# Kernel tuning notes

Measured on AMD Instinct MI355X. Metric: run time of the kernel, lower is better.

Reference implementation:

```python
import jax, jax.numpy as jnp
import numpy as np

K = 16  # nsample for knn_point

def _bn(x, g, b):
    # inference-mode BatchNorm1d folded to per-channel affine (running stats 0/1)
    return x * g[None, :, None] + b[None, :, None]

def _knn(xyz, k):
    # xyz: [B,3,N] -> idx [B,N,k] of k nearest neighbors (squared L2)
    p = xyz.transpose(0, 2, 1)                                   # [B,N,3]
    sq = jnp.sum(p * p, axis=-1)                                 # [B,N]
    d = sq[:, :, None] + sq[:, None, :] - 2.0 * jnp.einsum('bnc,bmc->bnm', p, p)
    _, idx = jax.lax.top_k(-d, k)
    return idx

def _gather(hT, idx):
    # hT: [B,N,C], idx: [B,N,K] -> [B,N,K,C]
    return jax.vmap(lambda a, i: a[i])(hT, idx)

def setup_inputs():
    key = jax.random.key(0)
    ks = jax.random.split(key, 12)
    B, N, C = 16, 2048, 128
    def w(k, shape, fan):
        return jax.random.normal(k, shape, jnp.float32) * (1.0 / np.sqrt(fan))
    o = jnp.ones; z = jnp.zeros
    return {
        'points': jax.random.normal(ks[0], (B, 6, N), jnp.float32),
        'label': jax.random.uniform(ks[1], (B, 1, 16), jnp.float32),
        'We1': w(ks[2], (C, 6), 6), 'ge1': o(C), 'be1': z(C),
        'We2': w(ks[3], (C, C), C), 'ge2': o(C), 'be2': z(C),
        'W1': w(ks[4], (3, C, C), C), 'g1': o((3, C)), 'b1': z((3, C)),
        'W2': w(ks[5], (3, C, C), C), 'g2': o((3, C)), 'b2': z((3, C)),
        'Wf': w(ks[6], (1024, 3 * C), 3 * C), 'gf': o(1024), 'bf': z(1024),
        'Wl': w(ks[7], (64, 16), 16), 'gl': o(64), 'bl': z(64),
        'Wc1': w(ks[8], (512, 3136), 3136), 'bc1': z(512), 'gc1': o(512), 'bb1': z(512),
        'Wc2': w(ks[9], (256, 512), 512), 'bc2': z(256), 'gc2': o(256), 'bb2': z(256),
        'Wc3': w(ks[10], (50, 256), 256), 'bc3': z(50),
    }

def reference(points, label, We1, ge1, be1, We2, ge2, be2, W1, g1, b1, W2, g2, b2,
              Wf, gf, bf, Wl, gl, bl, Wc1, bc1, gc1, bb1, Wc2, bc2, gc2, bb2, Wc3, bc3):
    B, _, N = points.shape
    x = points[:, :6, :]
    xyz = x[:, :3, :]
    idx = _knn(xyz, K)                                            # [B,N,16]
    # input embedding: two conv1x1 + BN + ReLU
    h = jax.nn.relu(_bn(jnp.einsum('oc,bcn->bon', We1, x), ge1, be1))
    h = jax.nn.relu(_bn(jnp.einsum('oc,bcn->bon', We2, h), ge2, be2))
    xs = []
    for i in range(3):  # PVDSA_Res blocks (simplified: conv-BN-ReLU, kNN max-agg, conv-BN + residual)
        t = jax.nn.relu(_bn(jnp.einsum('oc,bcn->bon', W1[i], h), g1[i], b1[i]))
        nbr = _gather(t.transpose(0, 2, 1), idx)                  # [B,N,K,C]
        m = nbr.max(axis=2).transpose(0, 2, 1)                    # [B,C,N]
        h = jax.nn.relu(_bn(jnp.einsum('oc,bcn->bon', W2[i], m), g2[i], b2[i]) + h)
        xs.append(h)
    xcat = jnp.concatenate(xs, axis=1)                            # [B,384,N]
    xf = jax.nn.leaky_relu(_bn(jnp.einsum('oc,bcn->bon', Wf, xcat), gf, bf), 0.2)  # [B,1024,N]
    x_max = xf.max(axis=-1)                                       # [B,1024]
    x_avg = xf.mean(axis=-1)                                      # [B,1024]
    cls = jnp.broadcast_to(label.transpose(0, 2, 1), (B, 16, N))
    lab = jax.nn.leaky_relu(_bn(jnp.einsum('oc,bcn->bon', Wl, cls), gl, bl), 0.2)  # [B,64,N]
    glob = jnp.concatenate([
        jnp.broadcast_to(x_max[:, :, None], (B, 1024, N)),
        jnp.broadcast_to(x_avg[:, :, None], (B, 1024, N)),
        lab], axis=1)
    xa = jnp.concatenate([xf, glob], axis=1)                      # [B,3136,N]
    c = jax.nn.relu(_bn(jnp.einsum('oc,bcn->bon', Wc1, xa) + bc1[None, :, None], gc1, bb1))
    c = jax.nn.relu(_bn(jnp.einsum('oc,bcn->bon', Wc2, c) + bc2[None, :, None], gc2, bb2))
    out = jnp.einsum('oc,bcn->bon', Wc3, c) + bc3[None, :, None]  # [B,50,N]
    return out
```

## Files before the change

kernel.cpp:

```cpp
#include <hip/hip_runtime.h>
#include <cstdint>
#include <cstddef>

#define DEVINL __device__ __forceinline__

typedef float    f32x4 __attribute__((ext_vector_type(4)));
typedef _Float16 f16x8 __attribute__((ext_vector_type(8)));
typedef _Float16 f16x4 __attribute__((ext_vector_type(4)));
typedef short    s16x8 __attribute__((ext_vector_type(8)));

constexpr int BB = 16, NN = 2048, MM = 32768;

constexpr size_t OFF_WE1 = 0;
constexpr size_t OFF_WE2 = OFF_WE1 + 128 * 64 * 2;
constexpr size_t OFF_W1  = OFF_WE2 + 128 * 128 * 2;
constexpr size_t OFF_W2  = OFF_W1  + 3 * 128 * 128 * 2;
constexpr size_t OFF_WF  = OFF_W2  + 3 * 128 * 128 * 2;
constexpr size_t OFF_WC1 = OFF_WF  + 1024 * 384 * 2;
constexpr size_t OFF_WC2 = OFF_WC1 + 512 * 1024 * 2;
constexpr size_t OFF_WC3 = OFF_WC2 + 256 * 512 * 2;
constexpr size_t OFF_BC2 = OFF_WC3 + 128 * 256 * 2;
constexpr size_t OFF_BC3 = OFF_BC2 + 256 * 4;
constexpr size_t OFF_CVEC= OFF_BC3 + 128 * 4;
constexpr size_t OFF_PMAX= OFF_CVEC+ 16 * 512 * 4;
// ... 450 lines not shown
    for (int a = 0; a < 4; ++a)
#pragma unroll
        for (int c = 0; c < 2; ++c) acc1[a][c] = (f32x4){0.f, 0.f, 0.f, 0.f};
#pragma unroll
    for (int kt = 0; kt < 2; ++kt)
#pragma unroll
        for (int ks = 0; ks < 2; ++ks) {
            f16x8 af[4], bf[2];
#pragma unroll
            for (int oi = 0; oi < 4; ++oi) {
                const int row = oh + oi * 16 + r;
                const int slot = (ks * 4 + quad) ^ (row & 7);
                af[oi] = *(const f16x8*)(Aa + kt * 8192 + row * 64 + slot * 8);
            }
#pragma unroll
            for (int mi = 0; mi < 2; ++mi) {
                const int row = mh + mi * 16 + r;
                const int slot = (ks * 4 + quad) ^ (row & 7);
                bf[mi] = *(const f16x8*)(Bm + kt * 4096 + row * 64 + slot * 8);
            }
#pragma unroll
            for (int oi = 0; oi < 4; ++oi)
#pragma unroll
                for (int mi = 0; mi < 2; ++mi)
                    acc1[oi][mi] = __builtin_amdgcn_mfma_f32_16x16x32_f16(af[oi], bf[mi], acc1[oi][mi], 0, 0, 0);
        }
    __syncthreads();

    if constexpr (HAS_G2) {
#pragma unroll
        for (int kt = 0; kt < 2; ++kt)
#pragma unroll
            for (int t = 0; t < 4; ++t) {
                const int row = t * 32 + srow;
                const int gk = kt * 64 + ((sslot ^ (row & 7)) << 3);
                __builtin_amdgcn_global_load_lds(
                    (const __attribute__((address_space(1))) unsigned int*)(Wb + (size_t)row * 128 + gk),
                    (__attribute__((address_space(3))) unsigned int*)(Ab + kt * 8192 + t * 2048 + wave * 512),
                    16, 0, 0);
            }
    }

#pragma unroll
    for (int oi = 0; oi < 4; ++oi) {
        const int ol = oh + oi * 16 + quad * 4;
        const f32x4 bv = *(const f32x4*)(ba + ol);
        const int kt = ol >> 6, kk = ol & 63;
        const int chunk = kk >> 3, within = kk & 7;
#pragma unroll
        for (int mi = 0; mi < 2; ++mi) {
            const int row = mh + mi * 16 + r;
            f32x4 v = acc1[oi][mi] + bv;
            f16x4 rr = *(const f16x4*)(Res + (size_t)(m_blk + row) * ldR + roff + ol);
#pragma unroll
            for (int j = 0; j < 4; ++j) v[j] += (float)rr[j];
            f16x4 ov;
#pragma unroll
            for (int j = 0; j < 4; ++j) { float x = v[j]; ov[j] = (_Float16)((x > 0.f) ? x : 0.f); }
            *(f16x4*)(By1 + kt * 4096 + row * 64 + ((chunk ^ (row & 7)) << 3) + within) = ov;
        }
    }
    __syncthreads();

#pragma unroll
    for (int it = 0; it < 4; ++it) {
        const int g = it * 256 + tid;
        const int row = g >> 4, c = g & 15;
        const int kt = c >> 3, cc = c & 7;
        f16x8 o8 = *(const f16x8*)(By1 + kt * 4096 + row * 64 + ((cc ^ (row & 7)) << 3));
        *(f16x8*)(Y1 + (size_t)(m_blk + row) * 384 + yoff1 + c * 8) = o8;
    }

    if constexpr (HAS_G2) {
        f32x4 acc2[4][2];
#pragma unroll
        for (int a = 0; a < 4; ++a)
#pragma unroll
            for (int c = 0; c < 2; ++c) acc2[a][c] = (f32x4){0.f, 0.f, 0.f, 0.f};
#pragma unroll
        for (int kt = 0; kt < 2; ++kt)
#pragma unroll
            for (int ks = 0; ks < 2; ++ks) {
                f16x8 af[4], bf[2];
#pragma unroll
                for (int oi = 0; oi < 4; ++oi) {
                    const int row = oh + oi * 16 + r;
                    const int slot = (ks * 4 + quad) ^ (row & 7);
                    af[oi] = *(const f16x8*)(Ab + kt * 8192 + row * 64 + slot * 8);
                }
#pragma unroll
                for (int mi = 0; mi < 2; ++mi) {
                    const int row = mh + mi * 16 + r;
                    const int slot = (ks * 4 + quad) ^ (row & 7);
                    bf[mi] = *(const f16x8*)(By1 + kt * 4096 + row * 64 + slot * 8);
                }
#pragma unroll
                for (int oi = 0; oi < 4; ++oi)
#pragma unroll
                    for (int mi = 0; mi < 2; ++mi)
                        acc2[oi][mi] = __builtin_amdgcn_mfma_f32_16x16x32_f16(af[oi], bf[mi], acc2[oi][mi], 0, 0, 0);
            }

#pragma unroll
        for (int oi = 0; oi < 4; ++oi) {
            const int ol = oh + oi * 16 + quad * 4;
            const f32x4 bv = *(const f32x4*)(bb + ol);
#pragma unroll
            for (int mi = 0; mi < 2; ++mi) {
                const int row = mh + mi * 16 + r;
                f32x4 v = acc2[oi][mi] + bv;
                f16x4 ov;
#pragma unroll
                for (int j = 0; j < 4; ++j) { float x = v[j]; ov[j] = (_Float16)((x > 0.f) ? x : 0.f); }
                const int s = ((ol >> 2) ^ (row & 31)) << 2;
                *(f16x4*)(OT2 + row * 128 + s) = ov;
            }
        }
        __syncthreads();
#pragma unroll
        for (int it2 = 0; it2 < 4; ++it2) {
            const int row = it2 * 16 + (tid >> 4);
            const int c = tid & 15;
            const int s0 = ((c * 2) ^ (row & 31)) << 2;
            const int s1 = ((c * 2 + 1) ^ (row & 31)) << 2;
            f16x4 a  = *(const f16x4*)(OT2 + row * 128 + s0);
            f16x4 b2 = *(const f16x4*)(OT2 + row * 128 + s1);
            f16x8 o8;
            o8[0] = a[0]; o8[1] = a[1]; o8[2] = a[2]; o8[3] = a[3];
            o8[4] = b2[0]; o8[5] = b2[1]; o8[6] = b2[2]; o8[7] = b2[3];
            *(f16x8*)(Y2 + (size_t)(m_blk + row) * 128 + c * 8) = o8;
        }
    }
}

__global__ __launch_bounds__(256) void c2c3_kernel(
    const _Float16* __restrict__ W2c, const _Float16* __restrict__ W3c,
    const _Float16* __restrict__ X, float* __restrict__ Y32,
    const float* __restrict__ b2v, const float* __restrict__ b3v)
{
    __shared__ _Float16 SH[36864];
    _Float16* As = SH;
    _Float16* Bs = SH + 16384;
    _Float16* Y1 = SH + 20480;

    const int tid = threadIdx.x;
    const int lane = tid & 63, w = tid >> 6;
    const int r = lane & 15, quad = lane >> 4;
    const int m_blk = blockIdx.x * 64;

    const int srow  = w * 8 + (lane >> 3);
    const int sslot = lane & 7;

    f32x4 acc1[4][4];
#pragma unroll
    for (int a = 0; a < 4; ++a)
#pragma unroll
        for (int c = 0; c < 4; ++c) acc1[a][c] = (f32x4){0.f, 0.f, 0.f, 0.f};

    for (int kt8 = 0; kt8 < 8; ++kt8) {
        const int k0 = kt8 << 6;
        __syncthreads();
#pragma unroll
        for (int t = 0; t < 8; ++t) {
            const int row = t * 32 + srow;
            const int gk = k0 + ((sslot ^ (row & 7)) << 3);
            __builtin_amdgcn_global_load_lds(
                (const __attribute__((address_space(1))) unsigned int*)(W2c + (size_t)row * 512 + gk),
                (__attribute__((address_space(3))) unsigned int*)(As + t * 2048 + w * 512),
                16, 0, 0);
        }
#pragma unroll
        for (int t = 0; t < 2; ++t) {
            const int row = t * 32 + srow;
            const int gk = k0 + ((sslot ^ (row & 7)) << 3);
            __builtin_amdgcn_global_load_lds(
                (const __attribute__((address_space(1))) unsigned int*)(X + (size_t)(m_blk + row) * 512 + gk),
                (__attribute__((address_space(3))) unsigned int*)(Bs + t * 2048 + w * 512),
                16, 0, 0);
        }
        __syncthreads();
#pragma unroll
        for (int ks = 0; ks < 2; ++ks) {
            f16x8 af[4], bf[4];
#pragma unroll
            for (int oi = 0; oi < 4; ++oi) {
                const int row = w * 64 + oi * 16 + r;
                const int slot = (ks * 4 + quad) ^ (row & 7);
                af[oi] = *(const f16x8*)(As + row * 64 + slot * 8);
            }
#pragma unroll
            for (int mi = 0; mi < 4; ++mi) {
                const int row = mi * 16 + r;
                const int slot = (ks * 4 + quad) ^ (row & 7);
                bf[mi] = *(const f16x8*)(Bs + row * 64 + slot * 8);
            }
#pragma unroll
            for (int oi = 0; oi < 4; ++oi)
#pragma unroll
                for (int mi = 0; mi < 4; ++mi)
                    acc1[oi][mi] = __builtin_amdgcn_mfma_f32_16x16x32_f16(af[oi], bf[mi], acc1[oi][mi], 0, 0, 0);
        }
    }
    __syncthreads();

#pragma unroll
    for (int kk2 = 0; kk2 < 2; ++kk2)
#pragma unroll
        for (int t = 0; t < 4; ++t) {
            const int row = t * 32 + srow;
            const int gk = (kk2 << 6) + ((sslot ^ (row & 7)) << 3);
            __builtin_amdgcn_global_load_lds(
                (const __attribute__((address_space(1))) unsigned int*)(W3c + (size_t)row * 256 + gk),
                (__attribute__((address_space(3))) unsigned int*)(As + kk2 * 8192 + t * 2048 + w * 512),
                16, 0, 0);
        }

#pragma unroll
    for (int oi = 0; oi < 4; ++oi) {
        const int ol = w * 64 + oi * 16 + quad * 4;
        const f32x4 bv = *(const f32x4*)(b2v + ol);
        const int kk = ol & 63;
        const int chunk = kk >> 3, within = kk & 7;
#pragma unroll
        for (int mi = 0; mi < 4; ++mi) {
            const int row = mi * 16 + r;
            f32x4 v = acc1[oi][mi] + bv;
            f16x4 ov;
#pragma unroll
            for (int j = 0; j < 4; ++j) { float x = v[j]; ov[j] = (_Float16)((x > 0.f) ? x : 0.f); }
            *(f16x4*)(Y1 + w * 4096 + row * 64 + ((chunk ^ (row & 7)) << 3) + within) = ov;
        }
    }
    __syncthreads();

    f32x4 acc2[2][4];
#pragma unroll
    for (int a = 0; a < 2; ++a)
#pragma unroll
        for (int c = 0; c < 4; ++c) acc2[a][c] = (f32x4){0.f, 0.f, 0.f, 0.f};

#pragma unroll
    for (int h = 0; h < 2; ++h) {
        if (h == 1) {
            __syncthreads();
#pragma unroll
            for (int kk2 = 0; kk2 < 2; ++kk2)
#pragma unroll
                for (int t = 0; t < 4; ++t) {
                    const int row = t * 32 + srow;
                    const int gk = ((2 + kk2) << 6) + ((sslot ^ (row & 7)) << 3);
                    __builtin_amdgcn_global_load_lds(
                        (const __attribute__((address_space(1))) unsigned int*)(W3c + (size_t)row * 256 + gk),
                        (__attribute__((address_space(3))) unsigned int*)(As + kk2 * 8192 + t * 2048 + w * 512),
                        16, 0, 0);
                }
            __syncthreads();
        }
#pragma unroll
        for (int kk2 = 0; kk2 < 2; ++kk2) {
            const int kt = h * 2 + kk2;
#pragma unroll
            for (int ks = 0; ks < 2; ++ks) {
                f16x8 af2[2], bf2[4];
#pragma unroll
                for (int oi2 = 0; oi2 < 2; ++oi2) {
                    const int row = w * 32 + oi2 * 16 + r;
                    const int slot = (ks * 4 + quad) ^ (row & 7);
                    af2[oi2] = *(const f16x8*)(As + kk2 * 8192 + row * 64 + slot * 8);
                }
#pragma unroll
                for (int mi = 0; mi < 4; ++mi) {
                    const int row = mi * 16 + r;
                    const int slot = (ks * 4 + quad) ^ (row & 7);
                    bf2[mi] = *(const f16x8*)(Y1 + kt * 4096 + row * 64 + slot * 8);
                }
#pragma unroll
                for (int oi2 = 0; oi2 < 2; ++oi2)
#pragma unroll
                    for (int mi = 0; mi < 4; ++mi)
                        acc2[oi2][mi] = __builtin_amdgcn_mfma_f32_16x16x32_f16(af2[oi2], bf2[mi], acc2[oi2][mi], 0, 0, 0);
            }
        }
    }

#pragma unroll
    for (int oi2 = 0; oi2 < 2; ++oi2) {
        const int og = w * 32 + oi2 * 16 + quad * 4;
        const f32x4 bv = *(const f32x4*)(b3v + og);
#pragma unroll
        for (int mi = 0; mi < 4; ++mi) {
            const int m = m_blk + mi * 16 + r;
            const int bidx = m >> 11, n = m & 2047;
            f32x4 v = acc2[oi2][mi] + bv;
#pragma unroll
            for (int j = 0; j < 4; ++j) {
                const int o = og + j;
                if (o < 50)
                    Y32[((size_t)(bidx * 50 + o) << 11) + n] = v[j];
            }
        }
    }
}

__global__ __launch_bounds__(512, 2) void gemm256(
    const _Float16* __restrict__ W, const _Float16* __restrict__ X,
    _Float16* __restrict__ Y, const float* __restrict__ bias,
    int Kp, int ldX, int ldY, int Opad, int act, int biasPerBatch,
    float* __restrict__ pmax, float* __restrict__ psum)
{
    constexpr int ASZ = 256 * 64;
    __shared__ _Float16 SH[65536];
    const int tid  = threadIdx.x;
    const int lane = tid & 63, wave = tid >> 6;
    const int r = lane & 15, quad = lane >> 4;
    const int wo = wave & 3, wm = wave >> 2;
    const int m_blk = blockIdx.x * 256, o_blk = blockIdx.y * 256;
    const int nt = Kp >> 6;

    f32x4 acc[4][8];
#pragma unroll
    for (int a = 0; a < 4; ++a)
#pragma unroll
        for (int c = 0; c < 8; ++c) acc[a][c] = (f32x4){0.f, 0.f, 0.f, 0.f};

    const int srow  = wave * 8 + (lane >> 3);
    const int sslot = lane & 7;

    auto STAGE = [&](int bufi, int k0) {
        _Float16* As = SH + bufi * (2 * ASZ);
        _Float16* Bs = As + ASZ;
#pragma unroll
        for (int t = 0; t < 4; ++t) {
            const int rowA = t * 64 + srow;
            const int gk = k0 + ((sslot ^ (rowA & 7)) << 3);
            const _Float16* gA = W + (size_t)(o_blk + rowA) * Kp + gk;
            __builtin_amdgcn_global_load_lds(
                (const __attribute__((address_space(1))) unsigned int*)gA,
                (__attribute__((address_space(3))) unsigned int*)(As + t * 4096 + wave * 512),
                16, 0, 0);
        }
#pragma unroll
        for (int t = 0; t < 4; ++t) {
            const int rowB = t * 64 + srow;
            const int gk = k0 + ((sslot ^ (rowB & 7)) << 3);
            const _Float16* gB = X + (size_t)(m_blk + rowB) * ldX + gk;
            __builtin_amdgcn_global_load_lds(
                (const __attribute__((address_space(1))) unsigned int*)gB,
                (__attribute__((address_space(3))) unsigned int*)(Bs + t * 4096 + wave * 512),
                16, 0, 0);
        }
    };

    STAGE(0, 0);
    int cur = 0;
    for (int t = 0; t < nt; ++t) {
        if (t + 1 < nt) {
            STAGE(cur ^ 1, (t + 1) << 6);
            asm volatile("s_waitcnt vmcnt(8)" ::: "memory");
        } else {
            asm volatile("s_waitcnt vmcnt(0)" ::: "memory");
        }
        __builtin_amdgcn_sched_barrier(0);
        __builtin_amdgcn_s_barrier();
        asm volatile("" ::: "memory");

        const _Float16* As = SH + cur * (2 * ASZ);
        const _Float16* Bs = As + ASZ;
        __builtin_amdgcn_s_setprio(1);
#pragma unroll
        for (int ks = 0; ks < 2; ++ks) {
            f16x8 af[4], bf[8];
#pragma unroll
            for (int oi = 0; oi < 4; ++oi) {
                const int row = (wo << 6) + (oi << 4) + r;
                const int slot = (ks * 4 + quad) ^ (row & 7);
                af[oi] = *(const f16x8*)(As + row * 64 + slot * 8);
            }
#pragma unroll
            for (int mi = 0; mi < 8; ++mi) {
                const int row = (wm << 7) + (mi << 4) + r;
                const int slot = (ks * 4 + quad) ^ (row & 7);
                bf[mi] = *(const f16x8*)(Bs + row * 64 + slot * 8);
            }
#pragma unroll
            for (int oi = 0; oi < 4; ++oi)
#pragma unroll
                for (int mi = 0; mi < 8; ++mi)
                    acc[oi][mi] = __builtin_amdgcn_mfma_f32_16x16x32_f16(af[oi], bf[mi], acc[oi][mi], 0, 0, 0);
        }
        __builtin_amdgcn_s_setprio(0);
        asm volatile("" ::: "memory");
        __builtin_amdgcn_s_barrier();
        cur ^= 1;
    }
    __syncthreads();

    const int bb = biasPerBatch ? (m_blk >> 11) * Opad : 0;
    _Float16* OT = SH;
#pragma unroll
    for (int oi = 0; oi < 4; ++oi) {
        const int ol = (wo << 6) + (oi << 4) + (quad << 2);
        const f32x4 bv = *(const f32x4*)(bias + bb + o_blk + ol);
#pragma unroll
        for (int mi = 0; mi < 8; ++mi) {
            const int row = (wm << 7) + (mi << 4) + r;
            f32x4 v = acc[oi][mi] + bv;
            f16x4 ov;
#pragma unroll
            for (int j = 0; j < 4; ++j) {
                float x = v[j];
                if (act == 1)      x = (x > 0.f) ? x : 0.0f;
                else if (act == 2) x = (x > 0.f) ? x : 0.2f * x;
                ov[j] = (_Float16)x;
            }
            const int s = (ol >> 2) ^ (row & 31);
            *(f16x4*)(OT + row * 256 + s * 4) = ov;
        }
    }
    __syncthreads();
#pragma unroll
    for (int p2 = 0; p2 < 16; ++p2) {
        const int g = (p2 << 9) + tid;
        const int row = g >> 5, c = g & 31;
        const int s0 = ((c << 1)) ^ (row & 31);
        const int s1 = ((c << 1) | 1) ^ (row & 31);
        f16x4 a  = *(const f16x4*)(OT + row * 256 + s0 * 4);
        f16x4 b2 = *(const f16x4*)(OT + row * 256 + s1 * 4);
        f16x8 o8;
        o8[0] = a[0]; o8[1] = a[1]; o8[2] = a[2]; o8[3] = a[3];
        o8[4] = b2[0]; o8[5] = b2[1]; o8[6] = b2[2]; o8[7] = b2[3];
        *(f16x8*)(Y + (size_t)(m_blk + row) * ldY + o_blk + (c << 3)) = o8;
    }

    if (pmax) {
        const int cg = tid & 63, h8 = tid >> 6;
        float mx0 = -3.4e38f, mx1 = -3.4e38f, mx2 = -3.4e38f, mx3 = -3.4e38f;
        float sm0 = 0.f, sm1 = 0.f, sm2 = 0.f, sm3 = 0.f;
#pragma unroll
        for (int rr = 0; rr < 32; ++rr) {
            const int row = (h8 << 5) + rr;
            const f16x4 v = *(const f16x4*)(OT + row * 256 + ((cg ^ (row & 31)) << 2));
            const float x0 = (float)v[0], x1 = (float)v[1], x2 = (float)v[2], x3 = (float)v[3];
            mx0 = fmaxf(mx0, x0); sm0 += x0;
            mx1 = fmaxf(mx1, x1); sm1 += x1;
            mx2 = fmaxf(mx2, x2); sm2 += x2;
            mx3 = fmaxf(mx3, x3); sm3 += x3;
        }
        __syncthreads();
        float* PR = (float*)SH;
        float* pw = PR + (size_t)(((h8 << 8) + (cg << 2)) << 1);
        pw[0] = mx0; pw[1] = sm0; pw[2] = mx1; pw[3] = sm1;
        pw[4] = mx2; pw[5] = sm2; pw[6] = mx3; pw[7] = sm3;
        __syncthreads();
        if (tid < 256) {
            float M = -3.4e38f, S = 0.f;
#pragma unroll
            for (int h2 = 0; h2 < 8; ++h2) {
                M = fmaxf(M, PR[(size_t)(((h2 << 8) + tid) << 1)]);
                S += PR[(size_t)(((h2 << 8) + tid) << 1) + 1];
            }
            const int b2 = m_blk >> 11, mt = (m_blk >> 8) & 7;
            pmax[((size_t)((b2 << 3) + mt) << 10) + o_blk + tid] = M;
            psum[((size_t)((b2 << 3) + mt) << 10) + o_blk + tid] = S;
        }
    }
}

template<int TM>
__global__ __launch_bounds__(256) void gemm_tile(
    const _Float16* __restrict__ W, const _Float16* __restrict__ X,
    _Float16* __restrict__ Y, float* __restrict__ Y32,
    const float* __restrict__ bias, const _Float16* __restrict__ Res,
    int Kp, int ldX, int xoff, int ldY, int yoff, int Opad,
    int act, int biasPerBatch, int ldR, int roff, int Olimit)
{
    constexpr int MI = TM / 32;
    constexpr int ASZ = 128 * 64;
    constexpr int BSZ = TM * 64;
    __shared__ _Float16 SH[2 * (ASZ + BSZ)];

    const int tid  = threadIdx.x;
    const int lane = tid & 63, wave = tid >> 6;
    const int r = lane & 15, quad = lane >> 4;
    const int m_blk = blockIdx.x * TM, o_blk = blockIdx.y * 128;
    const int oh = (wave >> 1) * 64, mh = (wave & 1) * (TM / 2);

    f32x4 acc[4][MI];
#pragma unroll
    for (int a = 0; a < 4; ++a)
#pragma unroll
        for (int c = 0; c < MI; ++c) acc[a][c] = (f32x4){0.f, 0.f, 0.f, 0.f};

    const int srow  = wave * 8 + (lane >> 3);
    const int sslot = lane & 7;

    auto STAGE = [&](int bufi, int k0) {
        _Float16* As = SH + bufi * (ASZ + BSZ);
        _Float16* Bs = As + ASZ;
#pragma unroll
        for (int t = 0; t < 4; ++t) {
            const int rowA = t * 32 + srow;
            const int gk = k0 + ((sslot ^ (rowA & 7)) << 3);
            const _Float16* gA = W + (size_t)(o_blk + rowA) * Kp + gk;
            __builtin_amdgcn_global_load_lds(
                (const __attribute__((address_space(1))) unsigned int*)gA,
                (__attribute__((address_space(3))) unsigned int*)(As + t * 2048 + wave * 512),
                16, 0, 0);
        }
#pragma unroll
        for (int t = 0; t < TM / 32; ++t) {
            const int rowB = t * 32 + srow;
            const int gk = k0 + ((sslot ^ (rowB & 7)) << 3);
            const _Float16* gB = X + (size_t)(m_blk + rowB) * ldX + xoff + gk;
            __builtin_amdgcn_global_load_lds(
                (const __attribute__((address_space(1))) unsigned int*)gB,
                (__attribute__((address_space(3))) unsigned int*)(Bs + t * 2048 + wave * 512),
                16, 0, 0);
        }
    };

    const int nt = Kp >> 6;
    STAGE(0, 0);
    int cur = 0;
    for (int t = 0; t < nt; ++t) {
        if (t + 1 < nt) {
            STAGE(cur ^ 1, (t + 1) << 6);
            if constexpr (TM == 128) asm volatile("s_waitcnt vmcnt(8)" ::: "memory");
            else                     asm volatile("s_waitcnt vmcnt(6)" ::: "memory");
        } else {
            asm volatile("s_waitcnt vmcnt(0)" ::: "memory");
        }
        __builtin_amdgcn_sched_barrier(0);
        __builtin_amdgcn_s_barrier();
        asm volatile("" ::: "memory");

        const _Float16* As = SH + cur * (ASZ + BSZ);
        const _Float16* Bs = As + ASZ;
        __builtin_amdgcn_s_setprio(1);
#pragma unroll
        for (int ks = 0; ks < 2; ++ks) {
            f16x8 af[4], bf[MI];
#pragma unroll
            for (int oi = 0; oi < 4; ++oi) {
                const int row = oh + oi * 16 + r;
                const int slot = (ks * 4 + quad) ^ (row & 7);
                af[oi] = *(const f16x8*)(As + row * 64 + slot * 8);
            }
#pragma unroll
            for (int mi = 0; mi < MI; ++mi) {
                const int row = mh + mi * 16 + r;
                const int slot = (ks * 4 + quad) ^ (row & 7);
                bf[mi] = *(const f16x8*)(Bs + row * 64 + slot * 8);
            }
#pragma unroll
            for (int oi = 0; oi < 4; ++oi)
#pragma unroll
                for (int mi = 0; mi < MI; ++mi)
                    acc[oi][mi] = __builtin_amdgcn_mfma_f32_16x16x32_f16(af[oi], bf[mi], acc[oi][mi], 0, 0, 0);
        }
        __builtin_amdgcn_s_setprio(0);
        asm volatile("" ::: "memory");
        __builtin_amdgcn_s_barrier();
        cur ^= 1;
    }

    const int bb = biasPerBatch ? (m_blk >> 11) * Opad : 0;
    __syncthreads();

    if (Y32) {
#pragma unroll
        for (int oi = 0; oi < 4; ++oi) {
            const int og = o_blk + oh + oi * 16 + quad * 4;
            const f32x4 bv = *(const f32x4*)(bias + bb + og);
#pragma unroll
            for (int mi = 0; mi < MI; ++mi) {
                const int m = m_blk + mh + mi * 16 + r;
                const int bidx = m >> 11, n = m & 2047;
                f32x4 v = acc[oi][mi] + bv;
#pragma unroll
                for (int j = 0; j < 4; ++j) {
                    float x = v[j];
                    if (act == 1)      x = (x > 0.f) ? x : 0.0f;
                    else if (act == 2) x = (x > 0.f) ? x : 0.2f * x;
                    const int o = og + j;
                    if (o < Olimit)
                        Y32[((size_t)(bidx * 50 + o) << 11) + n] = x;
                }
            }
        }
        return;
    }

    _Float16* OT = SH;
#pragma unroll
    for (int oi = 0; oi < 4; ++oi) {
        const int ol = oh + oi * 16 + quad * 4;
        const f32x4 bv = *(const f32x4*)(bias + bb + o_blk + ol);
#pragma unroll
        for (int mi = 0; mi < MI; ++mi) {
            const int row = mh + mi * 16 + r;
            f32x4 v = acc[oi][mi] + bv;
            if (Res) {
                f16x4 rr = *(const f16x4*)(Res + (size_t)(m_blk + row) * ldR + roff + o_blk + ol);
#pragma unroll
                for (int j = 0; j < 4; ++j) v[j] += (float)rr[j];
            }
            f16x4 ov;
#pragma unroll
            for (int j = 0; j < 4; ++j) {
                float x = v[j];
                if (act == 1)      x = (x > 0.f) ? x : 0.0f;
                else if (act == 2) x = (x > 0.f) ? x : 0.2f * x;
                ov[j] = (_Float16)x;
            }
            const int s = ((ol >> 2) ^ (row & 31)) << 2;
            *(f16x4*)(OT + row * 128 + s) = ov;
        }
    }
    __syncthreads();
#pragma unroll
    for (int it2 = 0; it2 < TM / 16; ++it2) {
        const int row = it2 * 16 + (tid >> 4);
        const int c = tid & 15;
        const int s0 = ((c * 2) ^ (row & 31)) << 2;
        const int s1 = ((c * 2 + 1) ^ (row & 31)) << 2;
        f16x4 a = *(const f16x4*)(OT + row * 128 + s0);
        f16x4 b2 = *(const f16x4*)(OT + row * 128 + s1);
        f16x8 o8;
        o8[0] = a[0]; o8[1] = a[1]; o8[2] = a[2]; o8[3] = a[3];
        o8[4] = b2[0]; o8[5] = b2[1]; o8[6] = b2[2]; o8[7] = b2[3];
        *(f16x8*)(Y + (size_t)(m_blk + row) * ldY + yoff + o_blk + c * 8) = o8;
    }
}

__global__ __launch_bounds__(256) void cvec_kernel(
    const float* __restrict__ label, const float* __restrict__ Wl, const float* __restrict__ gl, const float* __restrict__ bl,
    const float* __restrict__ Wc1, const float* __restrict__ bc1, const float* __restrict__ gc1, const float* __restrict__ bb1,
    const float* __restrict__ pmax, const float* __restrict__ psum, float* __restrict__ cvec)
{
    __shared__ float v[2112];
    __shared__ float red[256];
    const int b = blockIdx.x, og = blockIdx.y, tid = threadIdx.x;
    for (int i = tid; i < 1024; i += 256) {
        float mx = -3.4e38f, sm = 0.f;
#pragma unroll
        for (int c = 0; c < 8; ++c) {
            mx = fmaxf(mx, pmax[((size_t)(b * 8 + c) << 10) + i]);
            sm += psum[((size_t)(b * 8 + c) << 10) + i];
        }
        v[i] = mx;
        v[1024 + i] = sm * (1.f / 2048.f);
    }
    if (tid < 64) {
        float s = 0.f;
        for (int i = 0; i < 16; ++i) s += Wl[tid * 16 + i] * label[b * 16 + i];
        s = gl[tid] * s + bl[tid];
        v[2048 + tid] = (s > 0.f) ? s : 0.2f * s;
    }
    __syncthreads();
    const int o = og * 64 + (tid >> 2), part = tid & 3;
    const float* wrow = Wc1 + (size_t)o * 3136 + 1024 + part * 528;
    float s = 0.f;
    for (int j = 0; j < 528; ++j) s += wrow[j] * v[part * 528 + j];
    red[tid] = s;
    __syncthreads();
    if (part == 0) {
        float tot = red[tid] + red[tid + 1] + red[tid + 2] + red[tid + 3];
        cvec[((size_t)b << 9) + o] = gc1[o] * (tot + bc1[o]) + bb1[o];
    }
}

extern "C" void kernel_launch(void* const* d_in, const int* in_sizes, int n_in,
                              void* d_out, int out_size, void* d_ws, size_t ws_size,
                              hipStream_t stream)
{
    (void)in_sizes; (void)n_in; (void)out_size; (void)ws_size;
    const float* points = (const float*)d_in[0];
    const float* label  = (const float*)d_in[1];
    const float* We1 = (const float*)d_in[2];
    const float* ge1 = (const float*)d_in[3];
    const float* be1 = (const float*)d_in[4];
    const float* We2 = (const float*)d_in[5];
    const float* ge2 = (const float*)d_in[6];
    const float* be2 = (const float*)d_in[7];
    const float* W1  = (const float*)d_in[8];
    const float* g1  = (const float*)d_in[9];
    const float* b1  = (const float*)d_in[10];
    const float* W2  = (const float*)d_in[11];
    const float* g2  = (const float*)d_in[12];
    const float* b2  = (const float*)d_in[13];
    const float* Wf  = (const float*)d_in[14];
    const float* gf  = (const float*)d_in[15];
    const float* bfv = (const float*)d_in[16];
    const float* Wl  = (const float*)d_in[17];
    const float* gl  = (const float*)d_in[18];
    const float* bl  = (const float*)d_in[19];
    const float* Wc1 = (const float*)d_in[20];
    const float* bc1 = (const float*)d_in[21];
    const float* gc1 = (const float*)d_in[22];
    const float* bb1 = (const float*)d_in[23];
    const float* Wc2 = (const float*)d_in[24];
    const float* bc2 = (const float*)d_in[25];
    const float* gc2 = (const float*)d_in[26];
    const float* bb2 = (const float*)d_in[27];
    const float* Wc3 = (const float*)d_in[28];
    const float* bc3 = (const float*)d_in[29];

    char* ws = (char*)d_ws;
    _Float16* hT  = (_Float16*)(ws + OFF_HT);
    _Float16* tT  = (_Float16*)(ws + OFF_TT);
    _Float16* tT2 = (_Float16*)(ws + OFF_MT);
    _Float16* xct = (_Float16*)(ws + OFF_XCAT);
    _Float16* xf  = (_Float16*)(ws + OFF_XF);
    _Float16* c1  = (_Float16*)(ws + OFF_C1);
    int*      idx = (int*)     (ws + OFF_IDX);
    _Float16* x0  = (_Float16*)(ws + OFF_X0);

    _Float16* wE1 = (_Float16*)(ws + OFF_WE1);
    _Float16* wE2 = (_Float16*)(ws + OFF_WE2);
    _Float16* w1f = (_Float16*)(ws + OFF_W1);
    _Float16* w2f = (_Float16*)(ws + OFF_W2);
    _Float16* wF  = (_Float16*)(ws + OFF_WF);
    _Float16* wC1 = (_Float16*)(ws + OFF_WC1);
    _Float16* wC2 = (_Float16*)(ws + OFF_WC2);
    _Float16* wC3 = (_Float16*)(ws + OFF_WC3);
    float* bC2 = (float*)(ws + OFF_BC2);
    float* bC3 = (float*)(ws + OFF_BC3);
    float* cv  = (float*)(ws + OFF_CVEC);
    float* pmx = (float*)(ws + OFF_PMAX);
    float* psm = (float*)(ws + OFF_PSUM);

    fold_all_kernel<<<dim3(4834), 256, 0, stream>>>(We1, ge1, We2, ge2, W1, g1, W2, g2,
                                                    Wf, gf, Wc1, gc1, Wc2, gc2, Wc3,
                                                    gc2, bc2, bb2, bc3, points, ws);
    knn_kernel<<<dim3(BB, NN / 32), 256, 0, stream>>>(points, idx);

    e12_kernel<<<dim3(512), 256, 0, stream>>>(wE1, wE2, x0, hT, be1, be2);

    gemm_tile<64><<<dim3(512, 1), 256, 0, stream>>>(w1f, hT, tT, nullptr, b1, nullptr,
                                                    128, 128, 0, 128, 0, 128, 1, 0, 0, 0, 128);

    pairg_kernel<true><<<dim3(512), 256, 0, stream>>>(w2f, w1f + 16384, (const short*)tT, idx, hT,
                                                      xct, tT2, b2, b1 + 128, 128, 0, 0);

    pairg_kernel<true><<<dim3(512), 256, 0, stream>>>(w2f + 16384, w1f + 2 * 16384, (const short*)tT2, idx, xct,
                                                      xct, tT, b2 + 128, b1 + 256, 384, 0, 128);

    pairg_kernel<false><<<dim3(512), 256, 0, stream>>>(w2f + 2 * 16384, nullptr, (const short*)tT, idx, xct,
                                                       xct, nullptr, b2 + 256, nullptr, 384, 128, 256);

    gemm256<<<dim3(128, 4), 512, 0, stream>>>(wF, xct, xf, bfv, 384, 384, 1024, 1024, 2, 0, pmx, psm);

    cvec_kernel<<<dim3(BB, 8), 256, 0, stream>>>(label, Wl, gl, bl, Wc1, bc1, gc1, bb1, pmx, psm, cv);

    gemm256<<<dim3(128, 2), 512, 0, stream>>>(wC1, xf, c1, cv, 1024, 1024, 512, 512, 1, 1, nullptr, nullptr);
// ... 4 lines not shown
```

Baseline: 366.7 us.

## Single-buffer gemm256 LDS and split epilogue to raise occupancy

```diff
diff --git a/kernel.cpp b/kernel.cpp
--- a/kernel.cpp
+++ b/kernel.cpp
@@ -776,14 +776,14 @@
     }
 }
 
-__global__ __launch_bounds__(512, 2) void gemm256(
+__global__ __launch_bounds__(512, 4) void gemm256(
     const _Float16* __restrict__ W, const _Float16* __restrict__ X,
     _Float16* __restrict__ Y, const float* __restrict__ bias,
     int Kp, int ldX, int ldY, int Opad, int act, int biasPerBatch,
     float* __restrict__ pmax, float* __restrict__ psum)
 {
     constexpr int ASZ = 256 * 64;
-    __shared__ _Float16 SH[65536];
+    __shared__ _Float16 SH[32768];
     const int tid  = threadIdx.x;
     const int lane = tid & 63, wave = tid >> 6;
     const int r = lane & 15, quad = lane >> 4;
@@ -799,48 +799,33 @@
 
     const int srow  = wave * 8 + (lane >> 3);
     const int sslot = lane & 7;
-
-    auto STAGE = [&](int bufi, int k0) {
-        _Float16* As = SH + bufi * (2 * ASZ);
-        _Float16* Bs = As + ASZ;
-#pragma unroll
-        for (int t = 0; t < 4; ++t) {
-            const int rowA = t * 64 + srow;
+    _Float16* As = SH;
+    _Float16* Bs = SH + ASZ;
+
+    for (int t = 0; t < nt; ++t) {
+        const int k0 = t << 6;
+        __syncthreads();
+#pragma unroll
+        for (int tt = 0; tt < 4; ++tt) {
+            const int rowA = tt * 64 + srow;
             const int gk = k0 + ((sslot ^ (rowA & 7)) << 3);
             const _Float16* gA = W + (size_t)(o_blk + rowA) * Kp + gk;
             __builtin_amdgcn_global_load_lds(
                 (const __attribute__((address_space(1))) unsigned int*)gA,
-                (__attribute__((address_space(3))) unsigned int*)(As + t * 4096 + wave * 512),
+                (__attribute__((address_space(3))) unsigned int*)(As + tt * 4096 + wave * 512),
                 16, 0, 0);
         }
 #pragma unroll
-        for (int t = 0; t < 4; ++t) {
-            const int rowB = t * 64 + srow;
+        for (int tt = 0; tt < 4; ++tt) {
+            const int rowB = tt * 64 + srow;
             const int gk = k0 + ((sslot ^ (rowB & 7)) << 3);
             const _Float16* gB = X + (size_t)(m_blk + rowB) * ldX + gk;
             __builtin_amdgcn_global_load_lds(
                 (const __attribute__((address_space(1))) unsigned int*)gB,
-                (__attribute__((address_space(3))) unsigned int*)(Bs + t * 4096 + wave * 512),
+                (__attribute__((address_space(3))) unsigned int*)(Bs + tt * 4096 + wave * 512),
                 16, 0, 0);
         }
-    };
-
-    STAGE(0, 0);
-    int cur = 0;
-    for (int t = 0; t < nt; ++t) {
-        if (t + 1 < nt) {
-            STAGE(cur ^ 1, (t + 1) << 6);
-            asm volatile("s_waitcnt vmcnt(8)" ::: "memory");
-        } else {
-            asm volatile("s_waitcnt vmcnt(0)" ::: "memory");
-        }
-        __builtin_amdgcn_sched_barrier(0);
-        __builtin_amdgcn_s_barrier();
-        asm volatile("" ::: "memory");
-
-        const _Float16* As = SH + cur * (2 * ASZ);
-        const _Float16* Bs = As + ASZ;
-        __builtin_amdgcn_s_setprio(1);
+        __syncthreads();
 #pragma unroll
         for (int ks = 0; ks < 2; ++ks) {
             f16x8 af[4], bf[8];
@@ -862,69 +847,72 @@
                 for (int mi = 0; mi < 8; ++mi)
                     acc[oi][mi] = __builtin_amdgcn_mfma_f32_16x16x32_f16(af[oi], bf[mi], acc[oi][mi], 0, 0, 0);
         }
-        __builtin_amdgcn_s_setprio(0);
-        asm volatile("" ::: "memory");
-        __builtin_amdgcn_s_barrier();
-        cur ^= 1;
     }
     __syncthreads();
 
     const int bb = biasPerBatch ? (m_blk >> 11) * Opad : 0;
     _Float16* OT = SH;
-#pragma unroll
-    for (int oi = 0; oi < 4; ++oi) {
-        const int ol = (wo << 6) + (oi << 4) + (quad << 2);
-        const f32x4 bv = *(const f32x4*)(bias + bb + o_blk + ol);
-#pragma unroll
-        for (int mi = 0; mi < 8; ++mi) {
-            const int row = (wm << 7) + (mi << 4) + r;
-            f32x4 v = acc[oi][mi] + bv;
-            f16x4 ov;
-#pragma unroll
-            for (int j = 0; j < 4; ++j) {
-                float x = v[j];
-                if (act == 1)      x = (x > 0.f) ? x : 0.0f;
-                else if (act == 2) x = (x > 0.f) ? x : 0.2f * x;
-                ov[j] = (_Float16)x;
-            }
-            const int s = (ol >> 2) ^ (row & 31);
-            *(f16x4*)(OT + row * 256 + s * 4) = ov;
-        }
-    }
-    __syncthreads();
-#pragma unroll
-    for (int p2 = 0; p2 < 16; ++p2) {
-        const int g = (p2 << 9) + tid;
-        const int row = g >> 5, c = g & 31;
-        const int s0 = ((c << 1)) ^ (row & 31);
-        const int s1 = ((c << 1) | 1) ^ (row & 31);
-        f16x4 a  = *(const f16x4*)(OT + row * 256 + s0 * 4);
-        f16x4 b2 = *(const f16x4*)(OT + row * 256 + s1 * 4);
-        f16x8 o8;
-        o8[0] = a[0]; o8[1] = a[1]; o8[2] = a[2]; o8[3] = a[3];
-        o8[4] = b2[0]; o8[5] = b2[1]; o8[6] = b2[2]; o8[7] = b2[3];
-        *(f16x8*)(Y + (size_t)(m_blk + row) * ldY + o_blk + (c << 3)) = o8;
+    const int cg = tid & 63, h8 = tid >> 6;
+    float pm0 = -3.4e38f, pm1 = -3.4e38f, pm2 = -3.4e38f, pm3 = -3.4e38f;
+    float ps0 = 0.f, ps1 = 0.f, ps2 = 0.f, ps3 = 0.f;
+#pragma unroll
+    for (int h = 0; h < 2; ++h) {
+        if (wm == h) {
+#pragma unroll
+            for (int oi = 0; oi < 4; ++oi) {
+                const int ol = (wo << 6) + (oi << 4) + (quad << 2);
+                const f32x4 bv = *(const f32x4*)(bias + bb + o_blk + ol);
+#pragma unroll
+                for (int mi = 0; mi < 8; ++mi) {
+                    const int rowl = (mi << 4) + r;
+                    f32x4 v = acc[oi][mi] + bv;
+                    f16x4 ov;
+#pragma unroll
+                    for (int j = 0; j < 4; ++j) {
+                        float x = v[j];
+                        if (act == 1)      x = (x > 0.f) ? x : 0.0f;
+                        else if (act == 2) x = (x > 0.f) ? x : 0.2f * x;
+                        ov[j] = (_Float16)x;
+                    }
+                    const int s = (ol >> 2) ^ (rowl & 31);
+                    *(f16x4*)(OT + rowl * 256 + s * 4) = ov;
+                }
+            }
+        }
+        __syncthreads();
+#pragma unroll
+        for (int p2 = 0; p2 < 8; ++p2) {
+            const int g = (p2 << 9) + tid;
+            const int rowl = g >> 5, c = g & 31;
+            const int s0 = ((c << 1)) ^ (rowl & 31);
+            const int s1 = ((c << 1) | 1) ^ (rowl & 31);
+            f16x4 a  = *(const f16x4*)(OT + rowl * 256 + s0 * 4);
+            f16x4 b2 = *(const f16x4*)(OT + rowl * 256 + s1 * 4);
+            f16x8 o8;
+            o8[0] = a[0]; o8[1] = a[1]; o8[2] = a[2]; o8[3] = a[3];
+            o8[4] = b2[0]; o8[5] = b2[1]; o8[6] = b2[2]; o8[7] = b2[3];
+            *(f16x8*)(Y + (size_t)(m_blk + (h << 7) + rowl) * ldY + o_blk + (c << 3)) = o8;
+        }
+        if (pmax) {
+#pragma unroll
+            for (int rr = 0; rr < 16; ++rr) {
+                const int rowl = (h8 << 4) + rr;
+                const f16x4 v = *(const f16x4*)(OT + rowl * 256 + ((cg ^ (rowl & 31)) << 2));
+                const float x0 = (float)v[0], x1 = (float)v[1], x2 = (float)v[2], x3 = (float)v[3];
+                pm0 = fmaxf(pm0, x0); ps0 += x0;
+                pm1 = fmaxf(pm1, x1); ps1 += x1;
+                pm2 = fmaxf(pm2, x2); ps2 += x2;
+                pm3 = fmaxf(pm3, x3); ps3 += x3;
+            }
+        }
+        __syncthreads();
     }
 
     if (pmax) {
-        const int cg = tid & 63, h8 = tid >> 6;
-        float mx0 = -3.4e38f, mx1 = -3.4e38f, mx2 = -3.4e38f, mx3 = -3.4e38f;
-        float sm0 = 0.f, sm1 = 0.f, sm2 = 0.f, sm3 = 0.f;
-#pragma unroll
-        for (int rr = 0; rr < 32; ++rr) {
-            const int row = (h8 << 5) + rr;
-            const f16x4 v = *(const f16x4*)(OT + row * 256 + ((cg ^ (row & 31)) << 2));
-            const float x0 = (float)v[0], x1 = (float)v[1], x2 = (float)v[2], x3 = (float)v[3];
-            mx0 = fmaxf(mx0, x0); sm0 += x0;
-            mx1 = fmaxf(mx1, x1); sm1 += x1;
-            mx2 = fmaxf(mx2, x2); sm2 += x2;
-            mx3 = fmaxf(mx3, x3); sm3 += x3;
-        }
-        __syncthreads();
         float* PR = (float*)SH;
         float* pw = PR + (size_t)(((h8 << 8) + (cg << 2)) << 1);
-        pw[0] = mx0; pw[1] = sm0; pw[2] = mx1; pw[3] = sm1;
-        pw[4] = mx2; pw[5] = sm2; pw[6] = mx3; pw[7] = sm3;
+        pw[0] = pm0; pw[1] = ps0; pw[2] = pm1; pw[3] = ps1;
+        pw[4] = pm2; pw[5] = ps2; pw[6] = pm3; pw[7] = ps3;
         __syncthreads();
         if (tid < 256) {
             float M = -3.4e38f, S = 0.f;
```

Result: slower. 850.7 us (+132.0%).
